# Optimization experiments

Hardware: AMD Instinct MI355X
Metric: run time of the kernel (lower is better)

Reference implementation:

```python
import jax, jax.numpy as jnp
import numpy as np

# Matcher cost weights (from __init__ defaults)
COST_CLASS, COST_BBOX, COST_GIOU, COST_MASK, COST_DICE = 2.0, 5.0, 2.0, 5.0, 5.0
EPS_DICE = 1e-5


def _cxcywh_to_xyxy(b):
    cx, cy, w, h = b[..., 0], b[..., 1], b[..., 2], b[..., 3]
    return jnp.stack([cx - 0.5 * w, cy - 0.5 * h, cx + 0.5 * w, cy + 0.5 * h], axis=-1)


def _generalized_box_iou(b1, b2):
    # b1: [N,4] xyxy, b2: [M,4] xyxy -> [N,M] pairwise GIoU
    area1 = (b1[:, 2] - b1[:, 0]) * (b1[:, 3] - b1[:, 1])  # [N]
    area2 = (b2[:, 2] - b2[:, 0]) * (b2[:, 3] - b2[:, 1])  # [M]
    lt = jnp.maximum(b1[:, None, :2], b2[None, :, :2])  # [N,M,2]
    rb = jnp.minimum(b1[:, None, 2:], b2[None, :, 2:])
    wh = jnp.clip(rb - lt, 0.0)
    inter = wh[..., 0] * wh[..., 1]
    union = area1[:, None] + area2[None, :] - inter
    iou = inter / union
    lt_e = jnp.minimum(b1[:, None, :2], b2[None, :, :2])
    rb_e = jnp.maximum(b1[:, None, 2:], b2[None, :, 2:])
    wh_e = jnp.clip(rb_e - lt_e, 0.0)
    area_e = wh_e[..., 0] * wh_e[..., 1]
    return iou - (area_e - union) / area_e


def setup_inputs() -> dict:
    key = jax.random.key(0)
    k1, k2, k3, k4, k5, k6 = jax.random.split(key, 6)
    B, Q, C, H, W = 4, 300, 81, 160, 160
    M, Hm, Wm = 400, 256, 256
    return {
        "pred_logits": jax.random.normal(k1, (B, Q, C), dtype=jnp.float32),
        "pred_boxes": jax.random.uniform(k2, (B, Q, 4), dtype=jnp.float32),
        "pred_masks": jax.random.normal(k3, (B, Q, H, W), dtype=jnp.float32),
        "tgt_boxes": jax.random.uniform(k4, (M, 4), dtype=jnp.float32),
        "tgt_masks": jax.random.uniform(k5, (M, Hm, Wm), dtype=jnp.float32),
        "tgt_ids": jax.random.randint(k6, (M,), 0, C, dtype=jnp.int64)
        if jax.config.jax_enable_x64 else jax.random.randint(k6, (M,), 0, C, dtype=jnp.int32),
    }


def reference(pred_logits, pred_boxes, pred_masks, tgt_boxes, tgt_masks, tgt_ids):
    B, Q = pred_logits.shape[:2]
    H, W = pred_masks.shape[-2:]
    P = H * W
    M = tgt_ids.shape[0]

    out_prob = jax.nn.softmax(pred_logits.reshape(B * Q, -1), axis=-1)  # [N,C]
    out_bbox = pred_boxes.reshape(B * Q, 4)                             # [N,4]
    mask_logits = pred_masks.reshape(B * Q, P)                          # [N,P]

    # bilinear resize of GT masks to prediction resolution (align_corners=False)
    tgt = jax.image.resize(tgt_masks, (M, H, W), method="bilinear").reshape(M, P)

    cost_class = -out_prob[:, tgt_ids]                                  # [N,M]
    cost_bbox = jnp.sum(jnp.abs(out_bbox[:, None, :] - tgt_boxes[None, :, :]), axis=-1)
    cost_giou = -_generalized_box_iou(_cxcywh_to_xyxy(out_bbox), _cxcywh_to_xyxy(tgt_boxes))

    # fused pairwise mean-BCE: -(log p @ t^T + log(1-p) @ (1-t)^T) / P
    log_p = jax.nn.log_sigmoid(mask_logits)
    log_1mp = jax.nn.log_sigmoid(-mask_logits)
    cost_mask = -(log_p @ tgt.T + log_1mp @ (1.0 - tgt).T) / P

    p = jax.nn.sigmoid(mask_logits)
    numerator = 2.0 * (p @ tgt.T)
    denominator = p.sum(-1)[:, None] + tgt.sum(-1)[None, :]
    cost_dice = 1.0 - (numerator + EPS_DICE) / (denominator + EPS_DICE)

    C = (COST_BBOX * cost_bbox + COST_GIOU * cost_giou + COST_CLASS * cost_class
         + COST_MASK * cost_mask + COST_DICE * cost_dice)
    return C.reshape(B, Q, M)
```

## Files before the change

### kernel.cpp

```cpp
#include <hip/hip_runtime.h>
#include <cstdint>

#define N_PRED 1200
#define M_TGT  400
#define KDIM   25600
#define NCLS   81
#define MPAD   448
#define KZN    25
#define NBLK   38
#define STEPS  16
#define TSLICE 28672

typedef __attribute__((ext_vector_type(8)))  short bf16x8;
typedef __attribute__((ext_vector_type(4)))  float f32x4;
typedef unsigned char uchar;

__device__ __forceinline__ ushort f2bf(float f) {
  union { float f; uint32_t u; } v; v.f = f;
  uint32_t u = v.u + 0x7fffu + ((v.u >> 16) & 1u);
  return (ushort)(u >> 16);
}

__device__ __forceinline__ float bf2f(ushort s) {
  union { uint32_t u; float f; } v; v.u = ((uint32_t)s) << 16;
  return v.f;
}

__device__ __forceinline__ uint32_t pk_fp8(float a, float b, float c, float d) {
  uint32_t v = (uint32_t)__builtin_amdgcn_cvt_pk_fp8_f32(a, b, 0, false);
  v = (uint32_t)__builtin_amdgcn_cvt_pk_fp8_f32(c, d, (int)v, true);
  return v;
}

__device__ __forceinline__ void gll16(const void* g, void* l) {
  __builtin_amdgcn_global_load_lds(
      (const __attribute__((address_space(1))) void*)g,
      (__attribute__((address_space(3))) void*)l, 16, 0, 0);
}

__global__ __launch_bounds__(256) void resize2(const float* __restrict__ tm,
                                               uchar* __restrict__ T,
                                               float* __restrict__ tsum) {
  __shared__ float rows[16][256];
  __shared__ float vbuf[8][256];

  int m = blockIdx.x, yt = blockIdx.y;
  int y0 = yt * 8;
  int t = threadIdx.x;

  int jbase = (int)ceilf((y0 + 0.5f) * 1.6f - 2.1f);

  const float* base = tm + (size_t)m * 65536;
  {
    int r = t >> 4;
    int c0 = (t & 15) * 16;
    int jr = min(max(jbase + r, 0), 255);
    const float4* src = reinterpret_cast<const float4*>(base + jr * 256 + c0);
#pragma unroll
    for (int i = 0; i < 4; ++i)
      *reinterpret_cast<float4*>(&rows[r][c0 + i * 4]) = src[i];
  }
  __syncthreads();

#pragma unroll
  for (int yy = 0; yy < 8; ++yy) {
    int y = y0 + yy;
    float s = (y + 0.5f) * 1.6f - 0.5f;
    int j0 = (int)ceilf(s - 1.6f);
    float w[4]; float wsum = 0.f;
#pragma unroll
    for (int a = 0; a < 4; ++a) {
      int j = j0 + a;
      float wv = fmaxf(0.f, 1.f - fabsf((float)j - s) * 0.625f);
      if (j < 0 || j > 255) wv = 0.f;
      w[a] = wv; wsum += wv;
    }
    float winv = __builtin_amdgcn_rcpf(wsum);
    float acc = 0.f;
    int rbase = j0 - jbase;
#pragma unroll
    for (int a = 0; a < 4; ++a) acc += w[a] * rows[rbase + a][t];
    vbuf[yy][t] = acc * winv;
  }
  __syncthreads();

  float bsum = 0.f;
  if (t < 160) {
    int yy = t / 20, ch = t - yy * 20;
    float o[8];
#pragma unroll
    for (int j = 0; j < 8; ++j) {
      int x = ch * 8 + j;
      float sx = (x + 0.5f) * 1.6f - 0.5f;
      int jx0 = (int)ceilf(sx - 1.6f);
      float wsum = 0.f, h = 0.f;
#pragma unroll
      for (int b = 0; b < 4; ++b) {
        int jj = jx0 + b;
        float wv = fmaxf(0.f, 1.f - fabsf((float)jj - sx) * 0.625f);
        if (jj < 0 || jj > 255) wv = 0.f;
        wsum += wv;
        h += wv * vbuf[yy][min(max(jj, 0), 255)];
      }
      h *= __builtin_amdgcn_rcpf(wsum);
      o[j] = h; bsum += h;
    }
    int p0 = (y0 + yy) * 160 + ch * 8;
    int kt = p0 >> 6, kq = (p0 >> 3) & 7;
    size_t a = ((size_t)(kt * 8 + kq) * MPAD + m) * 8;
    uint2 pk;
    pk.x = pk_fp8(o[0], o[1], o[2], o[3]);
    pk.y = pk_fp8(o[4], o[5], o[6], o[7]);
    *reinterpret_cast<uint2*>(&T[a]) = pk;
  }
#pragma unroll
  for (int o2 = 32; o2 > 0; o2 >>= 1) bsum += __shfl_down(bsum, o2, 64);
  __shared__ float red[4];
  int wid = t >> 6;
  if ((t & 63) == 0) red[wid] = bsum;
  __syncthreads();
  if (t == 0) atomicAdd(&tsum[m], red[0] + red[1] + red[2] + red[3]);
}

__global__ __launch_bounds__(512, 4) void gemm_mega(
    const float* __restrict__ pm, const uchar* __restrict__ Tg,
    ushort* __restrict__ part, float* __restrict__ SP, float* __restrict__ sump) {
  __shared__ uchar buf[2][TSLICE];
  __shared__ uchar abuf[2][2][32 * 72];

  int orig = blockIdx.x;
  int xcd = orig & 7, base = orig >> 3;
  int wgid = (xcd < 6 ? xcd * 119 : 714 + (xcd - 6) * 118) + base;
  int kz = wgid / NBLK;
  int bn = wgid - kz * NBLK;

  int t = threadIdx.x, lane = t & 63, w = t >> 6;
  int rg = w >> 2, cg = w & 3;
  int l15 = lane & 15, kq = lane >> 4;

  bool is_b = (t < 256);
  bool is_a = (t >= 256);

  int at = t & 255;
  int arow = at >> 3, kf = at & 7;
  int rowA = bn * 32 + arow;
  int rowAc = min(rowA, N_PRED - 1);
  const float* apf = pm + (size_t)rowAc * KDIM + kz * (STEPS * 64) + kf * 8;
  int awoff = arow * 72 + kf * 8;

  const uchar* tsrc = Tg + (size_t)(kz * STEPS) * TSLICE;
  int bbase = (kq * MPAD + cg * 112 + l15) * 8;
  int afbase = (rg * 16 + l15) * 72 + kq * 8;

  f32x4 z = {0.f, 0.f, 0.f, 0.f};
  f32x4 acc1[7], acc2[7];
#pragma unroll
  for (int j = 0; j < 7; ++j) { acc1[j] = z; acc2[j] = z; }
  float stx = 0.f, stp = 0.f;

  union fragu { uint2 u; long long l; };

#define WAITV(N) asm volatile("s_waitcnt vmcnt(" #N ")" ::: "memory")

#define STAGE_B(BI, ST)                                                        \
  do {                                                                         \
    const uchar* s_ = tsrc + (size_t)(ST) * TSLICE;                            \
    _Pragma("unroll")                                                          \
    for (int i_ = 0; i_ < 7; ++i_) {                                           \
      int c_ = w * 7 + i_;                                                     \
      gll16(s_ + c_ * 1024 + lane * 16, &buf[BI][c_ * 1024]);                  \
    }                                                                          \
  } while (0)

#define CONVERT(NI, V0, V1)                                                    \
  do {                                                                         \
    float xs_[8] = {V0.x, V0.y, V0.z, V0.w, V1.x, V1.y, V1.z, V1.w};           \
    uint32_t xw_[2], pw_[2];                                                   \
    _Pragma("unroll")                                                          \
    for (int h_ = 0; h_ < 2; ++h_) {                                           \
      float sg_[4];                                                            \
      _Pragma("unroll")                                                        \
      for (int q_ = 0; q_ < 4; ++q_) {                                         \
        float a_ = xs_[h_ * 4 + q_];                                           \
        float e_ = __expf(-fabsf(a_));                                         \
        float o_ = 1.f + e_;                                                   \
        float i_ = __builtin_amdgcn_rcpf(o_);                                  \
        sg_[q_] = (a_ >= 0.f) ? i_ : e_ * i_;                                  \
        stp += sg_[q_];                                                        \
        stx += fmaxf(a_, 0.f) + __logf(o_);                                    \
      }                                                                        \
      xw_[h_] = pk_fp8(xs_[h_ * 4], xs_[h_ * 4 + 1], xs_[h_ * 4 + 2], xs_[h_ * 4 + 3]); \
      pw_[h_] = pk_fp8(sg_[0], sg_[1], sg_[2], sg_[3]);                        \
    }                                                                          \
    *reinterpret_cast<uint2*>(&abuf[NI][0][awoff]) = make_uint2(xw_[0], xw_[1]); \
    *reinterpret_cast<uint2*>(&abuf[NI][1][awoff]) = make_uint2(pw_[0], pw_[1]); \
  } while (0)

#define ITER(ACUR, S)                                                          \
  do {                                                                         \
    if (is_a && (S) + 2 < STEPS) {     \
      float4 n0_ = *reinterpret_cast<const float4*>(apf + ((S) + 2) * 64);     \
      float4 n1_ = *reinterpret_cast<const float4*>(apf + ((S) + 2) * 64 + 4); \
      if (ACUR) { fB0 = n0_; fB1 = n1_; } else { fA0 = n0_; fA1 = n1_; }       \
    }                                                                          \
    if (is_b) WAITV(0);                   \
    __builtin_amdgcn_s_barrier();                                              \
    __builtin_amdgcn_sched_barrier(0);                                         \
    if ((S) + 1 < STEPS) {                                                     \
      if (is_b) STAGE_B(ACUR ^ 1, (S) + 1);                                    \
      if (is_a) { if (ACUR) CONVERT(0, fA0, fA1); else CONVERT(1, fB0, fB1); } \
    }                                                                          \
    _Pragma("unroll")                                                          \
    for (int h_ = 0; h_ < 2; ++h_) {                                           \
      fragu ax_, ap_;                                                          \
      ax_.u = *reinterpret_cast<const uint2*>(&abuf[ACUR][0][afbase + h_ * 32]); \
      ap_.u = *reinterpret_cast<const uint2*>(&abuf[ACUR][1][afbase + h_ * 32]); \
      __builtin_amdgcn_s_setprio(1);                                           \
      _Pragma("unroll")                                                        \
      for (int j_ = 0; j_ < 7; ++j_) {                                         \
        fragu bv_;                                                             \
        bv_.u = *reinterpret_cast<const uint2*>(                               \
            &buf[ACUR][bbase + h_ * 14336 + j_ * 128]);                        \
        acc1[j_] = __builtin_amdgcn_mfma_f32_16x16x32_fp8_fp8(ax_.l, bv_.l, acc1[j_], 0, 0, 0); \
        acc2[j_] = __builtin_amdgcn_mfma_f32_16x16x32_fp8_fp8(ap_.l, bv_.l, acc2[j_], 0, 0, 0); \
      }                                                                        \
      __builtin_amdgcn_s_setprio(0);                                           \
    }                                                                          \
    asm volatile("s_waitcnt lgkmcnt(0)" ::: "memory");                         \
  } while (0)

  float4 fA0, fA1, fB0, fB1;
  if (is_b) STAGE_B(0, 0);
  if (is_a) {
    float4 f00 = *reinterpret_cast<const float4*>(apf);
    float4 f01 = *reinterpret_cast<const float4*>(apf + 4);
    fB0 = *reinterpret_cast<const float4*>(apf + 64);
    fB1 = *reinterpret_cast<const float4*>(apf + 68);
    CONVERT(0, f00, f01);
  }
  asm volatile("s_waitcnt lgkmcnt(0)" ::: "memory");

  for (int s = 0; s < STEPS; s += 2) {
    ITER(0, s);
    ITER(1, s + 1);
  }
#undef ITER
#undef CONVERT
#undef STAGE_B
#undef WAITV

  if (is_a) {
    stx += __shfl_xor(stx, 1, 8); stx += __shfl_xor(stx, 2, 8); stx += __shfl_xor(stx, 4, 8);
    stp += __shfl_xor(stp, 1, 8); stp += __shfl_xor(stp, 2, 8); stp += __shfl_xor(stp, 4, 8);
    if ((at & 7) == 0 && rowA < N_PRED) {
      atomicAdd(SP + rowA, stx);
      atomicAdd(sump + rowA, stp);
    }
  }

  ushort* p1 = part;
  ushort* p2 = part + (size_t)KZN * 1200 * MPAD;
#pragma unroll
  for (int j = 0; j < 7; ++j)
#pragma unroll
    for (int rr = 0; rr < 4; ++rr) {
      int gn = bn * 32 + rg * 16 + kq * 4 + rr;
      if (gn < N_PRED) {
        int gm = cg * 112 + j * 16 + l15;
        size_t o = ((size_t)gn * KZN + kz) * MPAD + gm;
        p1[o] = f2bf(acc1[j][rr]);
        p2[o] = f2bf(acc2[j][rr]);
      }
    }
}

__global__ void probs_kernel(const float* __restrict__ logits, float* __restrict__ probs) {
  int n = blockIdx.x;
  int l = threadIdx.x;
  const float* row = logits + n * NCLS;
  float v0 = row[l];
  bool has2 = (l + 64) < NCLS;
  float v1 = has2 ? row[l + 64] : -3.4e38f;
  float mx = fmaxf(v0, v1);
#pragma unroll
  for (int o = 1; o < 64; o <<= 1) mx = fmaxf(mx, __shfl_xor(mx, o, 64));
  float e0 = expf(v0 - mx);
  float e1 = has2 ? expf(v1 - mx) : 0.f;
  float sm = e0 + e1;
#pragma unroll
  for (int o = 1; o < 64; o <<= 1) sm += __shfl_xor(sm, o, 64);
  float inv = 1.f / sm;
  probs[n * NCLS + l] = e0 * inv;
  if (has2) probs[n * NCLS + l + 64] = e1 * inv;
}

__global__ void combine2(const ushort* __restrict__ part,
                         const float* __restrict__ SP, const float* __restrict__ sump,
                         const float* __restrict__ tsum, const float* __restrict__ probs,
                         const float* __restrict__ pboxes, const float* __restrict__ tboxes,
                         const int* __restrict__ tids, float* __restrict__ out) {
  int idx = blockIdx.x * 256 + threadIdx.x;
  int n = idx / M_TGT;
  int m = idx - n * M_TGT;

  const ushort* p1 = part + (size_t)n * (KZN * MPAD) + m;
  const ushort* p2 = p1 + (size_t)KZN * 1200 * MPAD;
  float A1 = 0.f, A2 = 0.f;
  for (int kz = 0; kz < KZN; ++kz) {
    A1 += bf2f(p1[kz * MPAD]);
    A2 += bf2f(p2[kz * MPAD]);
  }
  float cm = (SP[n] - A1) * (1.0f / (float)KDIM);
  float cd = 1.f - (2.f * A2 + 1e-5f) / (sump[n] + tsum[m] + 1e-5f);
  float cc = -probs[n * NCLS + tids[m]];

  float4 pb = reinterpret_cast<const float4*>(pboxes)[n];
  float4 tb = reinterpret_cast<const float4*>(tboxes)[m];
  float l1 = fabsf(pb.x - tb.x) + fabsf(pb.y - tb.y) + fabsf(pb.z - tb.z) + fabsf(pb.w - tb.w);
  float px1 = pb.x - 0.5f * pb.z, py1 = pb.y - 0.5f * pb.w;
  float px2 = pb.x + 0.5f * pb.z, py2 = pb.y + 0.5f * pb.w;
  float tx1 = tb.x - 0.5f * tb.z, ty1 = tb.y - 0.5f * tb.w;
  float tx2 = tb.x + 0.5f * tb.z, ty2 = tb.y + 0.5f * tb.w;
  float a1 = (px2 - px1) * (py2 - py1);
  float a2 = (tx2 - tx1) * (ty2 - ty1);
  float iw = fmaxf(fminf(px2, tx2) - fmaxf(px1, tx1), 0.f);
  float ih = fmaxf(fminf(py2, ty2) - fmaxf(py1, ty1), 0.f);
  float inter = iw * ih;
  float uni = a1 + a2 - inter;
  float iou = inter / uni;
  float ew = fmaxf(fmaxf(px2, tx2) - fminf(px1, tx1), 0.f);
  float eh = fmaxf(fmaxf(py2, ty2) - fminf(py1, ty1), 0.f);
  float ae = ew * eh;
  float giou = iou - (ae - uni) / ae;

  out[idx] = 5.f * l1 + 2.f * (-giou) + 2.f * cc + 5.f * cm + 5.f * cd;
}


__device__ __forceinline__ float sigf(float x) {
  return 1.f / (1.f + __expf(-x));
}

__global__ void resize_lin(const float* __restrict__ tm, ushort* __restrict__ T,
                           float* __restrict__ tsum) {
  int m = blockIdx.x;
  int p = blockIdx.y * 256 + threadIdx.x;
  int y = p / 160;
  int x = p - y * 160;
  float wy[4], wx[4];
  int jy0, jx0;
  {
    float s = (y + 0.5f) * 1.6f - 0.5f;
    jy0 = (int)ceilf(s - 1.6f);
    float ws = 0.f;
#pragma unroll
    for (int a = 0; a < 4; ++a) {
      int j = jy0 + a;
      float w = fmaxf(0.f, 1.f - fabsf((float)j - s) * 0.625f);
      if (j < 0 || j > 255) w = 0.f;
      wy[a] = w; ws += w;
    }
    float inv = 1.f / ws;
#pragma unroll
    for (int a = 0; a < 4; ++a) wy[a] *= inv;
  }
  {
    float s = (x + 0.5f) * 1.6f - 0.5f;
    jx0 = (int)ceilf(s - 1.6f);
    float ws = 0.f;
#pragma unroll
    for (int b = 0; b < 4; ++b) {
      int j = jx0 + b;
      float w = fmaxf(0.f, 1.f - fabsf((float)j - s) * 0.625f);
      if (j < 0 || j > 255) w = 0.f;
      wx[b] = w; ws += w;
    }
    float inv = 1.f / ws;
#pragma unroll
    for (int b = 0; b < 4; ++b) wx[b] *= inv;
  }
  const float* base = tm + (size_t)m * 65536;
  float acc = 0.f;
#pragma unroll
  for (int a = 0; a < 4; ++a) {
    int jy = min(max(jy0 + a, 0), 255);
    float wya = wy[a];
#pragma unroll
    for (int b = 0; b < 4; ++b) {
      int jx = min(max(jx0 + b, 0), 255);
      acc += wya * wx[b] * base[jy * 256 + jx];
    }
  }
  T[(size_t)m * KDIM + p] = f2bf(acc);
  float v = acc;
#pragma unroll
  for (int o = 32; o > 0; o >>= 1) v += __shfl_down(v, o, 64);
  __shared__ float red[4];
  int wid = threadIdx.x >> 6;
  if ((threadIdx.x & 63) == 0) red[wid] = v;
  __syncthreads();
  if (threadIdx.x == 0) atomicAdd(&tsum[m], red[0] + red[1] + red[2] + red[3]);
}

__global__ void stats_kernel(const float* __restrict__ pm, float* __restrict__ S,
                             float* __restrict__ sump) {
  int n = blockIdx.x;
  const float4* row = reinterpret_cast<const float4*>(pm + (size_t)n * KDIM);
  float ssp = 0.f, sp = 0.f;
  for (int i = threadIdx.x; i < KDIM / 4; i += 256) {
    float4 v = row[i];
    float xs[4] = {v.x, v.y, v.z, v.w};
#pragma unroll
    for (int j = 0; j < 4; ++j) {
      float x = xs[j];
      float e = __expf(-fabsf(x));
      float inv1pe = 1.f / (1.f + e);
      sp += (x >= 0.f) ? inv1pe : e * inv1pe;
      ssp += fmaxf(x, 0.f) + log1pf(e);
    }
  }
#pragma unroll
  for (int o = 32; o > 0; o >>= 1) {
    ssp += __shfl_down(ssp, o, 64);
    sp  += __shfl_down(sp, o, 64);
  }
  __shared__ float red[8];
  int wid = threadIdx.x >> 6;
  if ((threadIdx.x & 63) == 0) { red[wid] = ssp; red[4 + wid] = sp; }
  __syncthreads();
  if (threadIdx.x == 0) {
    S[n]    = -(red[0] + red[1] + red[2] + red[3]);
    sump[n] = red[4] + red[5] + red[6] + red[7];
  }
}

__device__ __forceinline__ bf16x8 load_frag_lin(const ushort* p) {
  union { ushort4 u[2]; bf16x8 f; } fr;
  fr.u[0] = *reinterpret_cast<const ushort4*>(p);
  fr.u[1] = *reinterpret_cast<const ushort4*>(p + 4);
  return fr.f;
}

__global__ __launch_bounds__(256) void gemm_fused(
    const float* __restrict__ pm, const ushort* __restrict__ T,
    ushort* __restrict__ part1, ushort* __restrict__ part2, int k_per) {
  __shared__ ushort Ax[64][40];
  __shared__ ushort Ap[64][40];
  __shared__ ushort Bs[64][40];
  int n0 = blockIdx.x * 64;
  int m0 = blockIdx.y * 64;
  int kz = blockIdx.z;
  int k_begin = kz * k_per;
  int t = threadIdx.x;
  int r = t >> 2;
  int q = t & 3;
  bool a_ok = (n0 + r) < N_PRED;
  bool b_ok = (m0 + r) < M_TGT;
  const float*  pA = pm + (size_t)(n0 + r) * KDIM + k_begin + q * 8;
  const ushort* pB = T  + (size_t)(m0 + r) * KDIM + k_begin + q * 8;
  int lane = t & 63;
  int w = t >> 6;
  int wr = (w >> 1) * 32;
  int wc = (w & 1) * 32;
  int lrow = lane & 15;
  int kc = (lane >> 4) * 8;
  f32x4 zero = {0.f, 0.f, 0.f, 0.f};
  f32x4 acc1[2][2] = {{zero, zero}, {zero, zero}};
  f32x4 acc2[2][2] = {{zero, zero}, {zero, zero}};
  int steps = k_per / 32;
  for (int kt = 0; kt < steps; ++kt) {
    __syncthreads();
    float4 f0 = {0.f,0.f,0.f,0.f}, f1 = {0.f,0.f,0.f,0.f};
    if (a_ok) {
      f0 = *reinterpret_cast<const float4*>(pA);
      f1 = *reinterpret_cast<const float4*>(pA + 4);
    }
    pA += 32;
    ushort4 xa, xb, pa, pb4;
    xa.x = f2bf(f0.x); xa.y = f2bf(f0.y); xa.z = f2bf(f0.z); xa.w = f2bf(f0.w);
    xb.x = f2bf(f1.x); xb.y = f2bf(f1.y); xb.z = f2bf(f1.z); xb.w = f2bf(f1.w);
    pa.x = f2bf(sigf(f0.x)); pa.y = f2bf(sigf(f0.y)); pa.z = f2bf(sigf(f0.z)); pa.w = f2bf(sigf(f0.w));
    pb4.x = f2bf(sigf(f1.x)); pb4.y = f2bf(sigf(f1.y)); pb4.z = f2bf(sigf(f1.z)); pb4.w = f2bf(sigf(f1.w));
    *reinterpret_cast<ushort4*>(&Ax[r][q * 8])     = xa;
    *reinterpret_cast<ushort4*>(&Ax[r][q * 8 + 4]) = xb;
    *reinterpret_cast<ushort4*>(&Ap[r][q * 8])     = pa;
    *reinterpret_cast<ushort4*>(&Ap[r][q * 8 + 4]) = pb4;
    union { uint4 u; ushort4 s[2]; } bv;
    bv.u = make_uint4(0, 0, 0, 0);
    if (b_ok) bv.u = *reinterpret_cast<const uint4*>(pB);
    pB += 32;
    *reinterpret_cast<ushort4*>(&Bs[r][q * 8])     = bv.s[0];
    *reinterpret_cast<ushort4*>(&Bs[r][q * 8 + 4]) = bv.s[1];
    __syncthreads();
    bf16x8 ax[2], ap[2], bb[2];
#pragma unroll
    for (int i = 0; i < 2; ++i) {
      ax[i] = load_frag_lin(&Ax[wr + i * 16 + lrow][kc]);
      ap[i] = load_frag_lin(&Ap[wr + i * 16 + lrow][kc]);
      bb[i] = load_frag_lin(&Bs[wc + i * 16 + lrow][kc]);
    }
#pragma unroll
    for (int i = 0; i < 2; ++i)
#pragma unroll
      for (int j = 0; j < 2; ++j) {
        acc1[i][j] = __builtin_amdgcn_mfma_f32_16x16x32_bf16(ax[i], bb[j], acc1[i][j], 0, 0, 0);
        acc2[i][j] = __builtin_amdgcn_mfma_f32_16x16x32_bf16(ap[i], bb[j], acc2[i][j], 0, 0, 0);
      }
  }
  int rowb = (lane >> 4) * 4;
  int col = lane & 15;
#pragma unroll
  for (int i = 0; i < 2; ++i)
#pragma unroll
    for (int j = 0; j < 2; ++j)
#pragma unroll
      for (int rr = 0; rr < 4; ++rr) {
        int gn = n0 + wr + i * 16 + rowb + rr;
        int gm = m0 + wc + j * 16 + col;
        if (gn < N_PRED && gm < M_TGT) {
          size_t o = (size_t)kz * 480000 + (size_t)gn * 400 + gm;
          part1[o] = f2bf(acc1[i][j][rr]);
          part2[o] = f2bf(acc2[i][j][rr]);
        }
      }
}

__global__ void combine_fb(const ushort* __restrict__ part1, const ushort* __restrict__ part2,
                           const float* __restrict__ S, const float* __restrict__ sump,
                           const float* __restrict__ tsum, const float* __restrict__ probs,
                           const float* __restrict__ pboxes, const float* __restrict__ tboxes,
                           const int* __restrict__ tids, float* __restrict__ out, int KZ) {
  int idx = blockIdx.x * 256 + threadIdx.x;
  int n = idx / M_TGT;
  int m = idx - n * M_TGT;
  float A1 = 0.f, A2 = 0.f;
  for (int kz = 0; kz < KZ; ++kz) {
    A1 += bf2f(part1[(size_t)kz * 480000 + idx]);
    A2 += bf2f(part2[(size_t)kz * 480000 + idx]);
  }
  float cm = -(A1 + S[n]) * (1.0f / (float)KDIM);
  float cd = 1.f - (2.f * A2 + 1e-5f) / (sump[n] + tsum[m] + 1e-5f);
  float cc = -probs[n * NCLS + tids[m]];
  float4 pb = reinterpret_cast<const float4*>(pboxes)[n];
  float4 tb = reinterpret_cast<const float4*>(tboxes)[m];
  float l1 = fabsf(pb.x - tb.x) + fabsf(pb.y - tb.y) + fabsf(pb.z - tb.z) + fabsf(pb.w - tb.w);
  float px1 = pb.x - 0.5f * pb.z, py1 = pb.y - 0.5f * pb.w;
  float px2 = pb.x + 0.5f * pb.z, py2 = pb.y + 0.5f * pb.w;
  float tx1 = tb.x - 0.5f * tb.z, ty1 = tb.y - 0.5f * tb.w;
  float tx2 = tb.x + 0.5f * tb.z, ty2 = tb.y + 0.5f * tb.w;
  float a1 = (px2 - px1) * (py2 - py1);
  float a2 = (tx2 - tx1) * (ty2 - ty1);
  float iw = fmaxf(fminf(px2, tx2) - fmaxf(px1, tx1), 0.f);
  float ih = fmaxf(fminf(py2, ty2) - fmaxf(py1, ty1), 0.f);
  float inter = iw * ih;
  float uni = a1 + a2 - inter;
  float iou = inter / uni;
  float ew = fmaxf(fmaxf(px2, tx2) - fminf(px1, tx1), 0.f);
  float eh = fmaxf(fmaxf(py2, ty2) - fminf(py1, ty1), 0.f);
  float ae = ew * eh;
  float giou = iou - (ae - uni) / ae;
  out[idx] = 5.f * l1 + 2.f * (-giou) + 2.f * cc + 5.f * cm + 5.f * cd;
}


extern "C" void kernel_launch(void* const* d_in, const int* in_sizes, int n_in,
                              void* d_out, int out_size, void* d_ws, size_t ws_size,
                              hipStream_t stream) {
  const float* logits = (const float*)d_in[0];
  const float* pboxes = (const float*)d_in[1];
  const float* pmasks = (const float*)d_in[2];
  const float* tboxes = (const float*)d_in[3];
  const float* tmasks = (const float*)d_in[4];
  const int*   tids   = (const int*)d_in[5];
  float* out = (float*)d_out;
  char* ws = (char*)d_ws;

  const size_t offT     = 0;
  const size_t offPart  = 24371200;
  const size_t offProbs = offPart + 53760000;
  const size_t offStats = offProbs + 390400;
  const size_t needNew  = offStats + 11200;

  if (ws_size >= needNew) {
    uchar* Tg    = (uchar*)(ws + offT);
    ushort* part = (ushort*)(ws + offPart);
    float* probs = (float*)(ws + offProbs);
    float* SP    = (float*)(ws + offStats);
    float* sump  = (float*)(ws + offStats + 4800);
    float* tsum  = (float*)(ws + offStats + 9600);

    hipMemsetAsync(SP, 0, 11200, stream);
    resize2<<<dim3(M_TGT, 20), 256, 0, stream>>>(tmasks, Tg, tsum);
    probs_kernel<<<N_PRED, 64, 0, stream>>>(logits, probs);
    gemm_mega<<<NBLK * KZN, 512, 0, stream>>>(pmasks, Tg, part, SP, sump);
    combine2<<<1875, 256, 0, stream>>>(part, SP, sump, tsum, probs,
                                       pboxes, tboxes, tids, out);
  } else {
    ushort* T     = (ushort*)ws;
    float*  probs = (float*)(ws + 20480000);
    float*  S     = (float*)(ws + 20868800);
    float*  sump  = (float*)(ws + 20873600);
    float*  tsum  = (float*)(ws + 20878400);
    ushort* part1 = (ushort*)(ws + 20880000);
    size_t need8 = 20880000ull + 2ull * 8 * 480000 * 2;
    int KZf = (ws_size >= need8) ? 8 : 1;
    ushort* part2 = part1 + (size_t)KZf * 480000;

    hipMemsetAsync(tsum, 0, M_TGT * sizeof(float), stream);
    resize_lin<<<dim3(M_TGT, 100), 256, 0, stream>>>(tmasks, T, tsum);
    probs_kernel<<<N_PRED, 64, 0, stream>>>(logits, probs);
    stats_kernel<<<N_PRED, 256, 0, stream>>>(pmasks, S, sump);
    gemm_fused<<<dim3(19, 7, KZf), 256, 0, stream>>>(pmasks, T, part1, part2, KDIM / KZf);
    combine_fb<<<1875, 256, 0, stream>>>(part1, part2, S, sump, tsum, probs,
                                         pboxes, tboxes, tids, out, KZf);
  }
}
```

Before: 141.6 us.

## Spread A-conversion over all threads, get sigmoid row sums from padded ones column

Changes the K split from 25 to 20 slices of 20 steps each, which makes 760 blocks spread evenly as 95 per XCD. Every one of the 512 threads now converts 4 prediction values, where before only the upper 256 converted 8 each, so the conversion work is balanced against the B-tile staging. The per-row sigmoid sum is dropped from the GEMM loop. Instead, padding column 400 of the fp8 target matrix is filled with 1.0 and the sum is read back from the sigmoid GEMM output by a small extra kernel. This trims VALU work and atomics, but the sigmoid sum now comes from fp8-quantised values accumulated through bf16 partials, and it adds two tiny launches.

Measured after the change: 139.3 us. About the same (-1.6%).

```diff
diff --git a/kernel.cpp b/kernel.cpp
--- a/kernel.cpp
+++ b/kernel.cpp
@@ -6,9 +6,9 @@
 #define KDIM   25600
 #define NCLS   81
 #define MPAD   448
-#define KZN    25
+#define KZN    20
 #define NBLK   38
-#define STEPS  16
+#define STEPS  20
 #define TSLICE 28672
 
 typedef __attribute__((ext_vector_type(8)))  short bf16x8;
@@ -122,15 +122,23 @@
   if (t == 0) atomicAdd(&tsum[m], red[0] + red[1] + red[2] + red[3]);
 }
 
+__global__ void ones_init(uchar* __restrict__ T) {
+  int i = blockIdx.x * 256 + threadIdx.x;
+  if (i < 3200) {
+    uint2 v; v.x = 0x38383838u; v.y = 0x38383838u;
+    *reinterpret_cast<uint2*>(&T[((size_t)i * MPAD + 400) * 8]) = v;
+  }
+}
+
 __global__ __launch_bounds__(512, 4) void gemm_mega(
     const float* __restrict__ pm, const uchar* __restrict__ Tg,
-    ushort* __restrict__ part, float* __restrict__ SP, float* __restrict__ sump) {
+    ushort* __restrict__ part, float* __restrict__ SP) {
   __shared__ uchar buf[2][TSLICE];
   __shared__ uchar abuf[2][2][32 * 72];
 
   int orig = blockIdx.x;
   int xcd = orig & 7, base = orig >> 3;
-  int wgid = (xcd < 6 ? xcd * 119 : 714 + (xcd - 6) * 118) + base;
+  int wgid = xcd * 95 + base;
   int kz = wgid / NBLK;
   int bn = wgid - kz * NBLK;
 
@@ -139,14 +147,12 @@
   int l15 = lane & 15, kq = lane >> 4;
 
   bool is_b = (t < 256);
-  bool is_a = (t >= 256);
-
-  int at = t & 255;
-  int arow = at >> 3, kf = at & 7;
+
+  int arow = t >> 4, kc4 = t & 15;
   int rowA = bn * 32 + arow;
   int rowAc = min(rowA, N_PRED - 1);
-  const float* apf = pm + (size_t)rowAc * KDIM + kz * (STEPS * 64) + kf * 8;
-  int awoff = arow * 72 + kf * 8;
+  const float* apf = pm + (size_t)rowAc * KDIM + kz * (STEPS * 64) + kc4 * 4;
+  int awoff = arow * 72 + kc4 * 4;
 
   const uchar* tsrc = Tg + (size_t)(kz * STEPS) * TSLICE;
   int bbase = (kq * MPAD + cg * 112 + l15) * 8;
@@ -156,7 +162,7 @@
   f32x4 acc1[7], acc2[7];
 #pragma unroll
   for (int j = 0; j < 7; ++j) { acc1[j] = z; acc2[j] = z; }
-  float stx = 0.f, stp = 0.f;
+  float stx = 0.f;
 
   union fragu { uint2 u; long long l; };
 
@@ -172,43 +178,37 @@
     }                                                                          \
   } while (0)
 
-#define CONVERT(NI, V0, V1)                                                    \
+#define CONVERT(NI, V)                                                         \
   do {                                                                         \
-    float xs_[8] = {V0.x, V0.y, V0.z, V0.w, V1.x, V1.y, V1.z, V1.w};           \
-    uint32_t xw_[2], pw_[2];                                                   \
+    float xs_[4] = {V.x, V.y, V.z, V.w};                                       \
+    float sg_[4];                                                              \
     _Pragma("unroll")                                                          \
-    for (int h_ = 0; h_ < 2; ++h_) {                                           \
-      float sg_[4];                                                            \
-      _Pragma("unroll")                                                        \
-      for (int q_ = 0; q_ < 4; ++q_) {                                         \
-        float a_ = xs_[h_ * 4 + q_];                                           \
-        float e_ = __expf(-fabsf(a_));                                         \
-        float o_ = 1.f + e_;                                                   \
-        float i_ = __builtin_amdgcn_rcpf(o_);                                  \
-        sg_[q_] = (a_ >= 0.f) ? i_ : e_ * i_;                                  \
-        stp += sg_[q_];                                                        \
-        stx += fmaxf(a_, 0.f) + __logf(o_);                                    \
-      }                                                                        \
-      xw_[h_] = pk_fp8(xs_[h_ * 4], xs_[h_ * 4 + 1], xs_[h_ * 4 + 2], xs_[h_ * 4 + 3]); \
-      pw_[h_] = pk_fp8(sg_[0], sg_[1], sg_[2], sg_[3]);                        \
+    for (int q_ = 0; q_ < 4; ++q_) {                                           \
+      float a_ = xs_[q_];                                                      \
+      float e_ = __expf(-fabsf(a_));                                           \
+      float o_ = 1.f + e_;                                                     \
+      float i_ = __builtin_amdgcn_rcpf(o_);                                    \
+      sg_[q_] = (a_ >= 0.f) ? i_ : e_ * i_;                                    \
+      stx += fmaxf(a_, 0.f) + __logf(o_);                                      \
     }                                                                          \
-    *reinterpret_cast<uint2*>(&abuf[NI][0][awoff]) = make_uint2(xw_[0], xw_[1]); \
-    *reinterpret_cast<uint2*>(&abuf[NI][1][awoff]) = make_uint2(pw_[0], pw_[1]); \
+    *reinterpret_cast<uint32_t*>(&abuf[NI][0][awoff]) =                        \
+        pk_fp8(xs_[0], xs_[1], xs_[2], xs_[3]);                                \
+    *reinterpret_cast<uint32_t*>(&abuf[NI][1][awoff]) =                        \
+        pk_fp8(sg_[0], sg_[1], sg_[2], sg_[3]);                                \
   } while (0)
 
 #define ITER(ACUR, S)                                                          \
   do {                                                                         \
-    if (is_a && (S) + 2 < STEPS) {     \
-      float4 n0_ = *reinterpret_cast<const float4*>(apf + ((S) + 2) * 64);     \
-      float4 n1_ = *reinterpret_cast<const float4*>(apf + ((S) + 2) * 64 + 4); \
-      if (ACUR) { fB0 = n0_; fB1 = n1_; } else { fA0 = n0_; fA1 = n1_; }       \
+    if (is_b) WAITV(0);               \
+    if ((S) + 2 < STEPS) {             \
+      float4 nv_ = *reinterpret_cast<const float4*>(apf + ((S) + 2) * 64);     \
+      if (ACUR) fB = nv_; else fA = nv_;                                       \
     }                                                                          \
-    if (is_b) WAITV(0);                   \
     __builtin_amdgcn_s_barrier();                                              \
     __builtin_amdgcn_sched_barrier(0);                                         \
     if ((S) + 1 < STEPS) {                                                     \
       if (is_b) STAGE_B(ACUR ^ 1, (S) + 1);                                    \
-      if (is_a) { if (ACUR) CONVERT(0, fA0, fA1); else CONVERT(1, fB0, fB1); } \
+      if (ACUR) CONVERT(0, fA); else CONVERT(1, fB);                           \
     }                                                                          \
     _Pragma("unroll")                                                          \
     for (int h_ = 0; h_ < 2; ++h_) {                                           \
@@ -229,14 +229,12 @@
     asm volatile("s_waitcnt lgkmcnt(0)" ::: "memory");                         \
   } while (0)
 
-  float4 fA0, fA1, fB0, fB1;
-  if (is_b) STAGE_B(0, 0);
-  if (is_a) {
-    float4 f00 = *reinterpret_cast<const float4*>(apf);
-    float4 f01 = *reinterpret_cast<const float4*>(apf + 4);
-    fB0 = *reinterpret_cast<const float4*>(apf + 64);
-    fB1 = *reinterpret_cast<const float4*>(apf + 68);
-    CONVERT(0, f00, f01);
+  float4 fA, fB;
+  {
+    float4 f0 = *reinterpret_cast<const float4*>(apf);
+    fB = *reinterpret_cast<const float4*>(apf + 64);
+    if (is_b) STAGE_B(0, 0);
+    CONVERT(0, f0);
   }
   asm volatile("s_waitcnt lgkmcnt(0)" ::: "memory");
 
@@ -249,14 +247,10 @@
 #undef STAGE_B
 #undef WAITV
 
-  if (is_a) {
-    stx += __shfl_xor(stx, 1, 8); stx += __shfl_xor(stx, 2, 8); stx += __shfl_xor(stx, 4, 8);
-    stp += __shfl_xor(stp, 1, 8); stp += __shfl_xor(stp, 2, 8); stp += __shfl_xor(stp, 4, 8);
-    if ((at & 7) == 0 && rowA < N_PRED) {
-      atomicAdd(SP + rowA, stx);
-      atomicAdd(sump + rowA, stp);
-    }
-  }
+  stx += __shfl_xor(stx, 1, 16); stx += __shfl_xor(stx, 2, 16);
+  stx += __shfl_xor(stx, 4, 16); stx += __shfl_xor(stx, 8, 16);
+  if ((t & 15) == 0 && rowA < N_PRED)
+    atomicAdd(SP + rowA, stx);
 
   ushort* p1 = part;
   ushort* p2 = part + (size_t)KZN * 1200 * MPAD;
@@ -272,6 +266,17 @@
         p2[o] = f2bf(acc2[j][rr]);
       }
     }
+}
+
+__global__ void sumprow(const ushort* __restrict__ part, float* __restrict__ sump) {
+  int n = blockIdx.x * 256 + threadIdx.x;
+  if (n < N_PRED) {
+    const ushort* p2 = part + (size_t)KZN * 1200 * MPAD + (size_t)n * KZN * MPAD + 400;
+    float s = 0.f;
+#pragma unroll
+    for (int kz = 0; kz < KZN; ++kz) s += bf2f(p2[kz * MPAD]);
+    sump[n] = s;
+  }
 }
 
 __global__ void probs_kernel(const float* __restrict__ logits, float* __restrict__ probs) {
@@ -591,8 +596,10 @@
 
     hipMemsetAsync(SP, 0, 11200, stream);
     resize2<<<dim3(M_TGT, 20), 256, 0, stream>>>(tmasks, Tg, tsum);
+    ones_init<<<13, 256, 0, stream>>>(Tg);
     probs_kernel<<<N_PRED, 64, 0, stream>>>(logits, probs);
-    gemm_mega<<<NBLK * KZN, 512, 0, stream>>>(pmasks, Tg, part, SP, sump);
+    gemm_mega<<<NBLK * KZN, 512, 0, stream>>>(pmasks, Tg, part, SP);
+    sumprow<<<5, 256, 0, stream>>>(part, sump);
     combine2<<<1875, 256, 0, stream>>>(part, SP, sump, tsum, probs,
                                        pboxes, tboxes, tids, out);
   } else {
```
